# Kernel optimization log

Hardware: AMD Instinct MI355X
Metric: run time of the kernel (lower is better)

## Reference

```python
import jax, jax.numpy as jnp
import numpy as np
from jax import lax

TOPK = 2


def setup_inputs() -> dict:
    key = jax.random.key(0)
    k1, k2, k3, k4 = jax.random.split(key, 4)
    B, T, D, E = 4, 2048, 1024, 8
    x = jax.random.normal(k1, (B, T, D), dtype=jnp.float32)
    gate_w = jax.random.normal(k2, (E, D), dtype=jnp.float32) * 0.02
    w_fc = jax.random.normal(k3, (E, 4 * D, D), dtype=jnp.float32) * 0.02
    w_proj = jax.random.normal(k4, (E, D, 4 * D), dtype=jnp.float32) * 0.02
    return {"x": x, "gate_w": gate_w, "w_fc": w_fc, "w_proj": w_proj}


def reference(x, gate_w, w_fc, w_proj):
    B, T, D = x.shape
    E = gate_w.shape[0]
    N = B * T
    xf = x.reshape(N, D)

    # gating
    gate_logits = xf @ gate_w.T                      # [N, E]
    gate_probs = jax.nn.softmax(gate_logits, axis=-1)
    routing_weights, expert_indices = lax.top_k(gate_probs, TOPK)  # [N, K]
    routing_weights = routing_weights / routing_weights.sum(axis=-1, keepdims=True)

    # combine weights per (token, expert); top-k indices are distinct per token
    hot = jax.nn.one_hot(expert_indices, E, dtype=xf.dtype)        # [N, K, E]
    comb = jnp.einsum('nke,nk->ne', hot, routing_weights)          # [N, E]
    tok_sel = hot.sum(axis=1)                                      # [N, E] in {0,1}
    expert_freq = tok_sel.mean(axis=0)                             # [E]

    # per-expert MLP (relu^2), accumulated over experts via scan
    def step(acc, xs):
        w1, w2, ce = xs                      # [4D,D], [D,4D], [N]
        h = jnp.square(jax.nn.relu(xf @ w1.T))   # [N, 4D]
        y = h @ w2.T                             # [N, D]
        return acc + ce[:, None] * y, None

    out, _ = lax.scan(step, jnp.zeros_like(xf), (w_fc, w_proj, comb.T))
    out = out.reshape(B, T, D)

    balance_loss = (gate_probs.mean(axis=0) * lax.stop_gradient(expert_freq)).sum() * E
    return out, balance_loss
```

## Files before the change

kernel.cpp:

```cpp
#include <hip/hip_runtime.h>
#include <hip/hip_bf16.h>

#define NTOK 8192
#define DDIM 1024
#define HDIM 4096
#define NEXP 8
#define NPAIR (NTOK * 2)
#define NMTILE 136
#define NPADROW (NPAIR + NEXP * 128)

typedef __attribute__((ext_vector_type(8))) short short8;
typedef __attribute__((ext_vector_type(4))) float floatx4;

__device__ __forceinline__ unsigned short f2bf(float f) {
  unsigned u = __float_as_uint(f);
  u += 0x7fffu + ((u >> 16) & 1u);
  return (unsigned short)(u >> 16);
}

__device__ __forceinline__ void async_copy16(const void* g, void* l) {
  __builtin_amdgcn_global_load_lds(
      (const __attribute__((address_space(1))) unsigned int*)g,
      (__attribute__((address_space(3))) unsigned int*)l, 16, 0, 0);
}

__global__ void cast_kernel(const float* __restrict__ src,
                            unsigned short* __restrict__ dst, int n4) {
  int i = blockIdx.x * 256 + threadIdx.x;
  if (i >= n4) return;
  const float4 v = ((const float4*)src)[i];
  ushort4 o;
  o.x = f2bf(v.x); o.y = f2bf(v.y); o.z = f2bf(v.z); o.w = f2bf(v.w);
  ((ushort4*)dst)[i] = o;
}

__global__ __launch_bounds__(256) void gating_kernel(
    const float* __restrict__ x, const float* __restrict__ gw,
    int* __restrict__ selE, float* __restrict__ selW,
    int* __restrict__ cnt, float* __restrict__ psum) {
  __shared__ float gws[NEXP * DDIM];
  __shared__ float pblk[4][NEXP];
  __shared__ int cblk[NEXP];
  const int t = threadIdx.x;
  for (int i = t; i < NEXP * DDIM; i += 256) gws[i] = gw[i];
  if (t < NEXP) cblk[t] = 0;
  __syncthreads();
  const int wv = t >> 6, lane = t & 63;
  const int tok = blockIdx.x * 4 + wv;
  double acc[NEXP];
#pragma unroll
  for (int e = 0; e < NEXP; e++) acc[e] = 0.0;
  const float* xr = x + (size_t)tok * DDIM;
  for (int i = lane; i < DDIM; i += 64) {
    double xv = (double)xr[i];
#pragma unroll
    for (int e = 0; e < NEXP; e++) acc[e] += xv * (double)gws[e * DDIM + i];
  }
#pragma unroll
  for (int e = 0; e < NEXP; e++)
    for (int off = 32; off > 0; off >>= 1) acc[e] += __shfl_xor(acc[e], off, 64);
  if (lane == 0) {
    double mx = acc[0];
    for (int e = 1; e < NEXP; e++) mx = acc[e] > mx ? acc[e] : mx;
    double p[NEXP], s = 0.0;
    for (int e = 0; e < NEXP; e++) { p[e] = exp(acc[e] - mx); s += p[e]; }
    int e1 = 0; double b1 = p[0];
    for (int e = 1; e < NEXP; e++) if (p[e] > b1) { b1 = p[e]; e1 = e; }
    int e2 = -1; double b2 = -1.0;
    for (int e = 0; e < NEXP; e++) if (e != e1 && p[e] > b2) { b2 = p[e]; e2 = e; }
    double rs = b1 + b2;
    selE[tok * 2 + 0] = e1; selE[tok * 2 + 1] = e2;
    selW[tok * 2 + 0] = (float)(b1 / rs); selW[tok * 2 + 1] = (float)(b2 / rs);
    atomicAdd(&cblk[e1], 1); atomicAdd(&cblk[e2], 1);
    for (int e = 0; e < NEXP; e++) pblk[wv][e] = (float)(p[e] / s);
  }
  __syncthreads();
  if (t < NEXP) {
    float sp = pblk[0][t] + pblk[1][t] + pblk[2][t] + pblk[3][t];
    atomicAdd(&psum[t], sp);
    if (cblk[t]) atomicAdd(&cnt[t], cblk[t]);
  }
}

__global__ __launch_bounds__(256) void finalize_kernel(
    const int* __restrict__ cnt, const float* __restrict__ psum,
    int* __restrict__ abase, int* __restrict__ fill,
    int* __restrict__ tile2exp, float* __restrict__ loss_out) {
  __shared__ int sb[NEXP + 1];
  __shared__ int scnt[NEXP];
  const int t = threadIdx.x;
  if (t == 0) {
    int b = 0;
    for (int e = 0; e < NEXP; e++) {
      int c = cnt[e];
      scnt[e] = c; sb[e] = b;
      b += ((c + 127) >> 7) << 7;
    }
    sb[NEXP] = b;
  }
  __syncthreads();
  if (t < NEXP) { abase[t] = sb[t]; fill[t] = sb[t]; }
  if (t == NEXP) abase[NEXP] = sb[NEXP];
  for (int i = t; i < NMTILE; i += 256) {
    int ex = -1;
#pragma unroll
    for (int e = 0; e < NEXP; e++) {
      int t0 = sb[e] >> 7, nt = (scnt[e] + 127) >> 7;
      if (i >= t0 && i < t0 + nt) ex = e;
    }
    tile2exp[i] = ex;
  }
  if (t == 0) {
    double L = 0.0;
    for (int e = 0; e < NEXP; e++) L += (double)psum[e] * (double)scnt[e];
    *loss_out = (float)(L * (double)NEXP / ((double)NTOK * (double)NTOK));
  }
}

__global__ __launch_bounds__(256) void scatter_kernel(
    const int* __restrict__ selE, const float* __restrict__ selW,
    int* __restrict__ fill, int* __restrict__ pairtok, float* __restrict__ pairw) {
  __shared__ int h1[NEXP], h2[NEXP], base[NEXP];
  const int t = threadIdx.x;
  if (t < NEXP) { h1[t] = 0; h2[t] = 0; }
  __syncthreads();
  const int n = blockIdx.x * 256 + t;
  const int e0 = selE[n * 2 + 0], e1 = selE[n * 2 + 1];
  atomicAdd(&h1[e0], 1); atomicAdd(&h1[e1], 1);
  __syncthreads();
  if (t < NEXP && h1[t]) base[t] = atomicAdd(&fill[t], h1[t]);
  __syncthreads();
  int r0 = atomicAdd(&h2[e0], 1);
  int p0 = base[e0] + r0;
  pairtok[p0] = n; pairw[p0] = selW[n * 2 + 0];
  int r1 = atomicAdd(&h2[e1], 1);
  int p1 = base[e1] + r1;
  pairtok[p1] = n; pairw[p1] = selW[n * 2 + 1];
}

template <int KD, int ND, int MODE>
__global__ __launch_bounds__(512, 1) void moe_gemm(
    const unsigned short* __restrict__ A, const unsigned short* __restrict__ B,
    const int* __restrict__ abase, const int* __restrict__ cnt,
    const int* __restrict__ tile2exp, const int* __restrict__ pairtok,
    const float* __restrict__ pairw, unsigned short* __restrict__ hbuf,
    float* __restrict__ out) {
  constexpr int NT = ND / 256;
  constexpr int KT = KD / 32;

  const int nwg = NT * NMTILE;
  const int lid = blockIdx.y * NT + blockIdx.x;
  const int q8 = nwg >> 3, r8 = nwg & 7;
  const int xcd = lid & 7, sub = lid >> 3;
  const int cbase = (xcd < r8) ? xcd * (q8 + 1) : r8 * (q8 + 1) + (xcd - r8) * q8;
  const int nlid = cbase + sub;
  const int mtile = nlid / NT;
  const int ntile = nlid - mtile * NT;

  const int e = tile2exp[mtile];
  if (e < 0) return;
  const int m0 = abase[e];
  const int cntE = cnt[e];
  const int mloc = mtile * 128 - m0;

  __shared__ unsigned short ldsA[4][512 * 8];
  __shared__ unsigned short ldsB[4][1024 * 8];

  const int t = threadIdx.x, w = t >> 6, lane = t & 63;

  const int cA = t;
  const int rowA = cA >> 2;
  const int qA = (cA & 3) ^ (rowA & 3) ^ ((rowA >> 2) & 3);
  int ar = mloc + rowA;
  if (ar > cntE - 1) ar = cntE - 1;
  size_t arow;
  if (MODE == 0) arow = (size_t)pairtok[m0 + ar];
  else           arow = (size_t)(m0 + ar);
  const unsigned short* gA = A + arow * (size_t)KD + qA * 8;
  const int dstAoff = (w * 64) * 8;

  const unsigned short* gB[2];
  int dstBoff[2];
#pragma unroll
  for (int i = 0; i < 2; i++) {
    const int p = i * 512 + t;
    const int rowB = p >> 2;
    const int qB = (p & 3) ^ (rowB & 3) ^ ((rowB >> 2) & 3);
    gB[i] = B + ((size_t)e * ND + (ntile * 256 + rowB)) * (size_t)KD + qB * 8;
    dstBoff[i] = (i * 512 + w * 64) * 8;
  }

  const int wr = w >> 2, wc = w & 3;
  const int sw = (lane >> 4) ^ (lane & 3) ^ ((lane >> 2) & 3);
  int apos[4], bpos[4];
#pragma unroll
  for (int i = 0; i < 4; i++) {
    apos[i] = (wr * 64 + i * 16 + (lane & 15)) * 4 + sw;
    bpos[i] = (wc * 64 + i * 16 + (lane & 15)) * 4 + sw;
  }

  floatx4 acc[4][4] = {};

  auto stage = [&](int kt2) {
    const int s = kt2 & 3;
    const int ko = kt2 * 32;
    async_copy16(gA + ko, &ldsA[s][dstAoff]);
    async_copy16(gB[0] + ko, &ldsB[s][dstBoff[0]]);
    async_copy16(gB[1] + ko, &ldsB[s][dstBoff[1]]);
  };

  stage(0);
  stage(1);
  asm volatile("s_waitcnt vmcnt(3)" ::: "memory");
  __builtin_amdgcn_s_barrier();

#pragma unroll 4
  for (int kt = 0; kt < KT; ++kt) {
    const int s = kt & 3;
    short8 a[4], b[4];
#pragma unroll
    for (int i = 0; i < 4; i++) {
      a[i] = ((const short8*)ldsA[s])[apos[i]];
      b[i] = ((const short8*)ldsB[s])[bpos[i]];
    }
    if (kt + 2 < KT) stage(kt + 2);
    __builtin_amdgcn_s_barrier();
    asm volatile("s_waitcnt lgkmcnt(0)" ::: "memory");
    __builtin_amdgcn_s_setprio(1);
#pragma unroll
    for (int im = 0; im < 4; im++)
#pragma unroll
      for (int in = 0; in < 4; in++)
        acc[im][in] = __builtin_amdgcn_mfma_f32_16x16x32_bf16(a[im], b[in], acc[im][in], 0, 0, 0);
    __builtin_amdgcn_s_setprio(0);
    if (kt + 2 < KT) asm volatile("s_waitcnt vmcnt(3)" ::: "memory");
    else             asm volatile("s_waitcnt vmcnt(0)" ::: "memory");
    __builtin_amdgcn_s_barrier();
  }

  const int Mv = cntE - mloc;
#pragma unroll
  for (int im = 0; im < 4; im++) {
#pragma unroll
    for (int r = 0; r < 4; r++) {
      const int rl = wr * 64 + im * 16 + (lane >> 4) * 4 + r;
      if (rl < Mv) {
        const int pr = m0 + mloc + rl;
        if (MODE == 0) {
#pragma unroll
          for (int in = 0; in < 4; in++) {
            float v = acc[im][in][r];
            v = v > 0.f ? v * v : 0.f;
            const int col = ntile * 256 + wc * 64 + in * 16 + (lane & 15);
            hbuf[(size_t)pr * HDIM + col] = f2bf(v);
          }
        } else {
          const float wgt = pairw[pr];
          const int tok = pairtok[pr];
          float* yrow = out + (size_t)tok * DDIM;
#pragma unroll
          for (int in = 0; in < 4; in++) {
            const int col = ntile * 256 + wc * 64 + in * 16 + (lane & 15);
            atomicAdd(yrow + col, wgt * acc[im][in][r]);
          }
        }
      }
    }
  }
}

extern "C" void kernel_launch(void* const* d_in, const int* in_sizes, int n_in,
                              void* d_out, int out_size, void* d_ws, size_t ws_size,
                              hipStream_t stream) {
  const float* x   = (const float*)d_in[0];
  const float* gw  = (const float*)d_in[1];
  const float* wfc = (const float*)d_in[2];
  const float* wpj = (const float*)d_in[3];
  float* out = (float*)d_out;

  char* ws = (char*)d_ws;
  size_t off = 0;
  auto alloc = [&](size_t bytes) -> void* {
    void* p = ws + off;
    off += (bytes + 255) & ~(size_t)255;
    return p;
  };
  unsigned short* xb   = (unsigned short*)alloc((size_t)NTOK * DDIM * 2);
  unsigned short* wfcb = (unsigned short*)alloc((size_t)NEXP * HDIM * DDIM * 2);
  unsigned short* wpjb = (unsigned short*)alloc((size_t)NEXP * DDIM * HDIM * 2);
  unsigned short* hbuf = (unsigned short*)alloc((size_t)NPADROW * HDIM * 2);
  int*   pairtok = (int*)alloc(NPADROW * 4);
  float* pairw   = (float*)alloc(NPADROW * 4);
  int*   selE    = (int*)alloc(NTOK * 2 * 4);
  float* selW    = (float*)alloc(NTOK * 2 * 4);
  int*   ctr     = (int*)alloc(1024);
  int* cnt = ctr; int* fill = ctr + 8; int* abase = ctr + 16;
  float* psum = (float*)(ctr + 28);
  int* tile2exp = ctr + 40;

  hipMemsetAsync(ctr, 0, 1024, stream);
  hipMemsetAsync(out, 0, (size_t)NTOK * DDIM * 4, stream);

  cast_kernel<<<(NTOK * DDIM / 4 + 255) / 256, 256, 0, stream>>>(x, xb, NTOK * DDIM / 4);
  cast_kernel<<<(NEXP * HDIM * DDIM / 4 + 255) / 256, 256, 0, stream>>>(wfc, wfcb, NEXP * HDIM * DDIM / 4);
  cast_kernel<<<(NEXP * DDIM * HDIM / 4 + 255) / 256, 256, 0, stream>>>(wpj, wpjb, NEXP * DDIM * HDIM / 4);

  gating_kernel<<<NTOK / 4, 256, 0, stream>>>(x, gw, selE, selW, cnt, psum);
  finalize_kernel<<<1, 256, 0, stream>>>(cnt, psum, abase, fill, tile2exp,
                                         out + (size_t)NTOK * DDIM);
  scatter_kernel<<<NTOK / 256, 256, 0, stream>>>(selE, selW, fill, pairtok, pairw);

  moe_gemm<DDIM, HDIM, 0><<<dim3(HDIM / 256, NMTILE), 512, 0, stream>>>(
      xb, wfcb, abase, cnt, tile2exp, pairtok, pairw, hbuf, nullptr);
  moe_gemm<HDIM, DDIM, 1><<<dim3(DDIM / 256, NMTILE), 512, 0, stream>>>(
      hbuf, wpjb, abase, cnt, tile2exp, pairtok, pairw, nullptr, out);
}
```

Measured before the change: 978.1 us.

## Use 256x256 GEMM tiles, split-K for down projection, deeper pipeline

Doubles the M tile from 128 to 256 rows, so each wave now computes 128x64 and the B tile is reused across twice as many rows. The second GEMM is split four ways along K through a grid z dimension, with partial sums accumulated by the existing atomics. This keeps enough workgroups despite the larger tiles. The LDS pipeline now prefetches three stages ahead and splits each k-step into two half-MMA phases, with the A and B loads interleaved. Risks are more padding waste per expert, a doubled accumulator register footprint that conflicts with the 2-blocks-per-SM launch bound, and four times as many atomic adds in the second GEMM.

Measured after the change: 893.5 us. 1.09x faster.

```diff
diff --git a/kernel.cpp b/kernel.cpp
--- a/kernel.cpp
+++ b/kernel.cpp
@@ -6,8 +6,8 @@
 #define HDIM 4096
 #define NEXP 8
 #define NPAIR (NTOK * 2)
-#define NMTILE 136
-#define NPADROW (NPAIR + NEXP * 128)
+#define NMT 72
+#define NPADROW (NPAIR + NEXP * 256)
 
 typedef __attribute__((ext_vector_type(8))) short short8;
 typedef __attribute__((ext_vector_type(4))) float floatx4;
@@ -94,18 +94,18 @@
     for (int e = 0; e < NEXP; e++) {
       int c = cnt[e];
       scnt[e] = c; sb[e] = b;
-      b += ((c + 127) >> 7) << 7;
+      b += ((c + 255) >> 8) << 8;
     }
     sb[NEXP] = b;
   }
   __syncthreads();
   if (t < NEXP) { abase[t] = sb[t]; fill[t] = sb[t]; }
   if (t == NEXP) abase[NEXP] = sb[NEXP];
-  for (int i = t; i < NMTILE; i += 256) {
+  for (int i = t; i < NMT; i += 256) {
     int ex = -1;
 #pragma unroll
     for (int e = 0; e < NEXP; e++) {
-      int t0 = sb[e] >> 7, nt = (scnt[e] + 127) >> 7;
+      int t0 = sb[e] >> 8, nt = (scnt[e] + 255) >> 8;
       if (i >= t0 && i < t0 + nt) ex = e;
     }
     tile2exp[i] = ex;
@@ -138,17 +138,17 @@
   pairtok[p1] = n; pairw[p1] = selW[n * 2 + 1];
 }
 
-template <int KD, int ND, int MODE>
-__global__ __launch_bounds__(512, 1) void moe_gemm(
+template <int KLEN, int KROW, int ND, int MODE>
+__global__ __launch_bounds__(512, 2) void moe_gemm(
     const unsigned short* __restrict__ A, const unsigned short* __restrict__ B,
     const int* __restrict__ abase, const int* __restrict__ cnt,
     const int* __restrict__ tile2exp, const int* __restrict__ pairtok,
     const float* __restrict__ pairw, unsigned short* __restrict__ hbuf,
     float* __restrict__ out) {
   constexpr int NT = ND / 256;
-  constexpr int KT = KD / 32;
-
-  const int nwg = NT * NMTILE;
+  constexpr int KT = KLEN / 32;
+
+  const int nwg = NT * NMT;
   const int lid = blockIdx.y * NT + blockIdx.x;
   const int q8 = nwg >> 3, r8 = nwg & 7;
   const int xcd = lid & 7, sub = lid >> 3;
@@ -161,108 +161,127 @@
   if (e < 0) return;
   const int m0 = abase[e];
   const int cntE = cnt[e];
-  const int mloc = mtile * 128 - m0;
-
-  __shared__ unsigned short ldsA[4][512 * 8];
-  __shared__ unsigned short ldsB[4][1024 * 8];
+  const int mloc = mtile * 256 - m0;
+  const int koff = blockIdx.z * KLEN;
+
+  __shared__ unsigned short lds[4][2][8192];
 
   const int t = threadIdx.x, w = t >> 6, lane = t & 63;
 
-  const int cA = t;
-  const int rowA = cA >> 2;
-  const int qA = (cA & 3) ^ (rowA & 3) ^ ((rowA >> 2) & 3);
-  int ar = mloc + rowA;
-  if (ar > cntE - 1) ar = cntE - 1;
-  size_t arow;
-  if (MODE == 0) arow = (size_t)pairtok[m0 + ar];
-  else           arow = (size_t)(m0 + ar);
-  const unsigned short* gA = A + arow * (size_t)KD + qA * 8;
-  const int dstAoff = (w * 64) * 8;
-
-  const unsigned short* gB[2];
-  int dstBoff[2];
-#pragma unroll
-  for (int i = 0; i < 2; i++) {
-    const int p = i * 512 + t;
-    const int rowB = p >> 2;
-    const int qB = (p & 3) ^ (rowB & 3) ^ ((rowB >> 2) & 3);
-    gB[i] = B + ((size_t)e * ND + (ntile * 256 + rowB)) * (size_t)KD + qB * 8;
-    dstBoff[i] = (i * 512 + w * 64) * 8;
+  const unsigned short* gsrc[4];
+  int dchunk[4];
+#pragma unroll
+  for (int i = 0; i < 4; i++) {
+    const int c = (i & 1) * 512 + t;
+    const int row = c >> 2;
+    const int q = (c & 3) ^ (row & 3) ^ ((row >> 2) & 3);
+    dchunk[i] = (i & 1) * 512 + w * 64;
+    if (i < 2) {
+      int ar = mloc + row;
+      if (ar > cntE - 1) ar = cntE - 1;
+      size_t arow = (MODE == 0) ? (size_t)pairtok[m0 + ar] : (size_t)(m0 + ar);
+      gsrc[i] = A + arow * (size_t)KROW + koff + q * 8;
+    } else {
+      gsrc[i] = B + ((size_t)e * ND + (ntile * 256 + row)) * (size_t)KROW + koff + q * 8;
+    }
   }
 
   const int wr = w >> 2, wc = w & 3;
   const int sw = (lane >> 4) ^ (lane & 3) ^ ((lane >> 2) & 3);
-  int apos[4], bpos[4];
-#pragma unroll
-  for (int i = 0; i < 4; i++) {
-    apos[i] = (wr * 64 + i * 16 + (lane & 15)) * 4 + sw;
-    bpos[i] = (wc * 64 + i * 16 + (lane & 15)) * 4 + sw;
-  }
-
-  floatx4 acc[4][4] = {};
-
-  auto stage = [&](int kt2) {
-    const int s = kt2 & 3;
-    const int ko = kt2 * 32;
-    async_copy16(gA + ko, &ldsA[s][dstAoff]);
-    async_copy16(gB[0] + ko, &ldsB[s][dstBoff[0]]);
-    async_copy16(gB[1] + ko, &ldsB[s][dstBoff[1]]);
-  };
-
-  stage(0);
-  stage(1);
-  asm volatile("s_waitcnt vmcnt(3)" ::: "memory");
+  int aoff[8], boff[4];
+#pragma unroll
+  for (int i = 0; i < 8; i++) aoff[i] = (wr * 128 + i * 16 + (lane & 15)) * 4 + sw;
+#pragma unroll
+  for (int i = 0; i < 4; i++) boff[i] = (wc * 64 + i * 16 + (lane & 15)) * 4 + sw;
+
+  floatx4 acc[8][4] = {};
+
+#pragma unroll
+  for (int p = 0; p < 3; ++p) {
+    unsigned short* d0 = &lds[p][0][0];
+    unsigned short* d1 = &lds[p][1][0];
+    async_copy16(gsrc[0] + p * 32, d0 + dchunk[0] * 8);
+    async_copy16(gsrc[1] + p * 32, d0 + dchunk[1] * 8);
+    async_copy16(gsrc[2] + p * 32, d1 + dchunk[2] * 8);
+    async_copy16(gsrc[3] + p * 32, d1 + dchunk[3] * 8);
+  }
+  asm volatile("s_waitcnt vmcnt(8)" ::: "memory");
   __builtin_amdgcn_s_barrier();
 
-#pragma unroll 4
-  for (int kt = 0; kt < KT; ++kt) {
-    const int s = kt & 3;
-    short8 a[4], b[4];
-#pragma unroll
-    for (int i = 0; i < 4; i++) {
-      a[i] = ((const short8*)ldsA[s])[apos[i]];
-      b[i] = ((const short8*)ldsB[s])[bpos[i]];
-    }
-    if (kt + 2 < KT) stage(kt + 2);
+  auto tile = [&](int kt, int vmw) __attribute__((always_inline)) {
+    const int s_ = kt & 3;
+    const short8* LA = (const short8*)(&lds[s_][0][0]);
+    const short8* LB = (const short8*)(&lds[s_][1][0]);
+    short8 af[4], bf[4];
+#pragma unroll
+    for (int i = 0; i < 4; i++) { af[i] = LA[aoff[i]]; bf[i] = LB[boff[i]]; }
+    if (kt + 3 < KT) {
+      unsigned short* d = &lds[(kt + 3) & 3][0][0];
+      async_copy16(gsrc[0] + (kt + 3) * 32, d + dchunk[0] * 8);
+      async_copy16(gsrc[1] + (kt + 3) * 32, d + dchunk[1] * 8);
+    }
     __builtin_amdgcn_s_barrier();
     asm volatile("s_waitcnt lgkmcnt(0)" ::: "memory");
     __builtin_amdgcn_s_setprio(1);
 #pragma unroll
-    for (int im = 0; im < 4; im++)
-#pragma unroll
-      for (int in = 0; in < 4; in++)
-        acc[im][in] = __builtin_amdgcn_mfma_f32_16x16x32_bf16(a[im], b[in], acc[im][in], 0, 0, 0);
+    for (int mi = 0; mi < 4; mi++)
+#pragma unroll
+      for (int ni = 0; ni < 4; ni++)
+        acc[mi][ni] = __builtin_amdgcn_mfma_f32_16x16x32_bf16(af[mi], bf[ni], acc[mi][ni], 0, 0, 0);
     __builtin_amdgcn_s_setprio(0);
-    if (kt + 2 < KT) asm volatile("s_waitcnt vmcnt(3)" ::: "memory");
-    else             asm volatile("s_waitcnt vmcnt(0)" ::: "memory");
     __builtin_amdgcn_s_barrier();
-  }
+    short8 ag[4];
+#pragma unroll
+    for (int i = 0; i < 4; i++) ag[i] = LA[aoff[4 + i]];
+    if (kt + 3 < KT) {
+      unsigned short* d = &lds[(kt + 3) & 3][1][0];
+      async_copy16(gsrc[2] + (kt + 3) * 32, d + dchunk[2] * 8);
+      async_copy16(gsrc[3] + (kt + 3) * 32, d + dchunk[3] * 8);
+    }
+    __builtin_amdgcn_s_barrier();
+    asm volatile("s_waitcnt lgkmcnt(0)" ::: "memory");
+    __builtin_amdgcn_s_setprio(1);
+#pragma unroll
+    for (int mi = 0; mi < 4; mi++)
+#pragma unroll
+      for (int ni = 0; ni < 4; ni++)
+        acc[4 + mi][ni] = __builtin_amdgcn_mfma_f32_16x16x32_bf16(ag[mi], bf[ni], acc[4 + mi][ni], 0, 0, 0);
+    __builtin_amdgcn_s_setprio(0);
+    if (vmw == 8)      asm volatile("s_waitcnt vmcnt(8)" ::: "memory");
+    else if (vmw == 4) asm volatile("s_waitcnt vmcnt(4)" ::: "memory");
+    else if (vmw == 0) asm volatile("s_waitcnt vmcnt(0)" ::: "memory");
+    __builtin_amdgcn_s_barrier();
+  };
+
+  for (int kt = 0; kt < KT - 3; ++kt) tile(kt, 8);
+  tile(KT - 3, 4);
+  tile(KT - 2, 0);
+  tile(KT - 1, -1);
 
   const int Mv = cntE - mloc;
-#pragma unroll
-  for (int im = 0; im < 4; im++) {
+  const int colb = ntile * 256 + wc * 64 + (lane & 15);
+  const int rowb = wr * 128 + ((lane >> 4) << 2);
+#pragma unroll
+  for (int mi = 0; mi < 8; mi++) {
 #pragma unroll
     for (int r = 0; r < 4; r++) {
-      const int rl = wr * 64 + im * 16 + (lane >> 4) * 4 + r;
+      const int rl = rowb + mi * 16 + r;
       if (rl < Mv) {
         const int pr = m0 + mloc + rl;
         if (MODE == 0) {
-#pragma unroll
-          for (int in = 0; in < 4; in++) {
-            float v = acc[im][in][r];
+          unsigned short* hrow = hbuf + (size_t)pr * HDIM + colb;
+#pragma unroll
+          for (int ni = 0; ni < 4; ni++) {
+            float v = acc[mi][ni][r];
             v = v > 0.f ? v * v : 0.f;
-            const int col = ntile * 256 + wc * 64 + in * 16 + (lane & 15);
-            hbuf[(size_t)pr * HDIM + col] = f2bf(v);
+            hrow[ni * 16] = f2bf(v);
           }
         } else {
           const float wgt = pairw[pr];
-          const int tok = pairtok[pr];
-          float* yrow = out + (size_t)tok * DDIM;
-#pragma unroll
-          for (int in = 0; in < 4; in++) {
-            const int col = ntile * 256 + wc * 64 + in * 16 + (lane & 15);
-            atomicAdd(yrow + col, wgt * acc[im][in][r]);
-          }
+          float* yrow = out + (size_t)pairtok[pr] * DDIM + colb;
+#pragma unroll
+          for (int ni = 0; ni < 4; ni++)
+            atomicAdd(yrow + ni * 16, wgt * acc[mi][ni][r]);
         }
       }
     }
@@ -310,8 +329,8 @@
                                          out + (size_t)NTOK * DDIM);
   scatter_kernel<<<NTOK / 256, 256, 0, stream>>>(selE, selW, fill, pairtok, pairw);
 
-  moe_gemm<DDIM, HDIM, 0><<<dim3(HDIM / 256, NMTILE), 512, 0, stream>>>(
+  moe_gemm<1024, 1024, HDIM, 0><<<dim3(HDIM / 256, NMT, 1), 512, 0, stream>>>(
       xb, wfcb, abase, cnt, tile2exp, pairtok, pairw, hbuf, nullptr);
-  moe_gemm<HDIM, DDIM, 1><<<dim3(DDIM / 256, NMTILE), 512, 0, stream>>>(
+  moe_gemm<1024, 4096, DDIM, 1><<<dim3(DDIM / 256, NMT, 4), 512, 0, stream>>>(
       hbuf, wpjb, abase, cnt, tile2exp, pairtok, pairw, nullptr, out);
 }
```
